# Optimization experiments

Measured on AMD Instinct MI355X. Metric: run time of the kernel, lower is better.

## Reference

```python
import jax, jax.numpy as jnp
import numpy as np

T, F, C, V, H, E, S = 256, 32, 8, 10000, 1024, 256, 512
PAD, BOS, EOS = 0, 1, 2


def setup_inputs() -> dict:
    key = jax.random.key(0)
    ks = jax.random.split(key, 16)
    sH = 1.0 / np.sqrt(H).astype(np.float32)
    inp = {
        'token_ctx': jax.random.normal(ks[0], (1, S, H), jnp.float32),
        'char_emb_w': jax.random.normal(ks[1], (V, E), jnp.float32) * 0.02,
        'enc_W_ih': jax.random.normal(ks[2], (3 * H, E), jnp.float32) * sH,
        'enc_W_hh': jax.random.normal(ks[3], (3 * H, H), jnp.float32) * sH,
        'enc_b_ih': jnp.zeros((3 * H,), jnp.float32),
        'enc_b_hh': jnp.zeros((3 * H,), jnp.float32),
        'dec_W_ih': jax.random.normal(ks[4], (3 * H, E), jnp.float32) * sH,
        'dec_W_hh': jax.random.normal(ks[5], (3 * H, H), jnp.float32) * sH,
        'dec_b_ih': jnp.zeros((3 * H,), jnp.float32),
        'dec_b_hh': jnp.zeros((3 * H,), jnp.float32),
        'out_W': jax.random.normal(ks[6], (V, H), jnp.float32) * sH,
        'out_b': jnp.zeros((V,), jnp.float32),
    }
    # (token_id, xtoken_idx, char_id) triples; every token 1..T has exactly C chars
    tok_ids = jnp.repeat(jnp.arange(1, T + 1, dtype=jnp.int32), C)
    xt_ids = jax.random.randint(ks[7], (T * C,), 0, S, jnp.int32)
    ch_ids = jax.random.randint(ks[8], (T * C,), 4, V, jnp.int32)  # avoid specials
    inp['in_sent_token_chars'] = jnp.stack([tok_ids, xt_ids, ch_ids], axis=-1)[None]
    gold = jax.random.randint(ks[9], (T * F,), 4, V, jnp.int32)  # no EOS -> full-length decode
    inp['out_chars'] = jnp.concatenate([jnp.array([BOS], jnp.int32), gold])[None]
    inp['max_tokens'] = T
    inp['max_form_len'] = F
    inp['use_teacher_forcing'] = 1
    return inp


def _gru_cell(x, h, W_ih, W_hh, b_ih, b_hh):
    # PyTorch GRU cell convention; x:[T,E], h:[T,H]
    gi = x @ W_ih.T + b_ih
    gh = h @ W_hh.T + b_hh
    i_r, i_z, i_n = jnp.split(gi, 3, axis=-1)
    h_r, h_z, h_n = jnp.split(gh, 3, axis=-1)
    r = jax.nn.sigmoid(i_r + h_r)
    z = jax.nn.sigmoid(i_z + h_z)
    n = jnp.tanh(i_n + r * h_n)
    return (1.0 - z) * n + z * h


def reference(token_ctx, char_emb_w, enc_W_ih, enc_W_hh, enc_b_ih, enc_b_hh,
              dec_W_ih, dec_W_hh, dec_b_ih, dec_b_hh, out_W, out_b,
              in_sent_token_chars, out_chars, max_tokens, max_form_len,
              use_teacher_forcing):
    Vout = out_b.shape[0]
    # ragged mask select per token id -> here every token has exactly C chars
    tc = in_sent_token_chars[0].reshape(max_tokens, -1, 3)  # [T, C, 3]
    chars = tc[:, :, 2]          # [T, C]
    xtoken_ids = tc[:, :, 1]     # [T, C]
    # enc_state = mean over the token's xtoken contexts
    h0 = jnp.mean(token_ctx[0][xtoken_ids], axis=1)  # [T, H]
    # ---- encoder GRU over the token's chars (batched over tokens) ----
    x_enc = char_emb_w[chars]  # [T, C, E]

    def enc_step(h, x):
        return _gru_cell(x, h, enc_W_ih, enc_W_hh, enc_b_ih, enc_b_hh), None

    h_enc, _ = jax.lax.scan(enc_step, h0, jnp.swapaxes(x_enc, 0, 1))  # [T, H]
    # ---- decoder GRU, max_form_len steps, teacher-forced, EOS freeze+pad ----
    # gold char for token t at step s is out_chars[0, t*F + s + 1]
    gold = out_chars[0, 1:1 + max_tokens * max_form_len].reshape(max_tokens, max_form_len)
    c0 = jnp.full((max_tokens,), out_chars[0, 0], dtype=out_chars.dtype)
    done0 = (c0 == EOS)
    last0 = jnp.zeros((max_tokens, Vout), jnp.float32)

    def dec_step(carry, g):
        h, c, done, last = carry
        x = char_emb_w[c]
        h_new = _gru_cell(x, h, dec_W_ih, dec_W_hh, dec_b_ih, dec_b_hh)
        s_new = h_new @ out_W.T + out_b
        score = jnp.where(done[:, None], last, s_new)  # pad with last score after EOS
        h = jnp.where(done[:, None], h, h_new)         # state frozen after EOS
        if use_teacher_forcing:
            c_next = g
        else:
            c_next = jnp.argmax(s_new, axis=-1).astype(c.dtype)
        done = done | (c_next == EOS)
        return (h, c_next, done, score), score

    _, scores = jax.lax.scan(dec_step, (h_enc, c0, done0, last0),
                             jnp.swapaxes(gold, 0, 1))  # [F, T, V]
    # torch.cat(dec_scores, dim=1): token-major, step-minor -> [1, T*F, V]
    return jnp.transpose(scores, (1, 0, 2)).reshape(1, max_tokens * max_form_len, Vout)
```

## Files before the change

### kernel.cpp

```cpp
#include <hip/hip_runtime.h>
#include <hip/hip_bf16.h>
#include <math.h>

#define TT   256
#define FF   32
#define CCH  8
#define VV   10000
#define HH   1024
#define EE   256
#define NG   3072
#define EOS_ID 2
#define NSTEPS 40
#define CHAIN_BLKS 256
#define CTR_INTS 512

#define LDS_B_BYTES   98304
#define LDS_GP_OFF    98304
#define LDS_STB_OFF   (98304 + 13312)
#define LDS_TOTAL     (98304 + 13312 + 2048)

typedef __attribute__((ext_vector_type(8))) short bf16x8;
typedef __attribute__((ext_vector_type(4))) float f32x4;

__device__ __forceinline__ void gload_lds16(const void* g, void* l) {
    __builtin_amdgcn_global_load_lds((const __attribute__((address_space(1))) void*)g,
                                     (__attribute__((address_space(3))) void*)l,
                                     16, 0, 0);
}

__device__ __forceinline__ float sigmf(float x) { return 1.f / (1.f + __expf(-x)); }

__global__ __launch_bounds__(256) void prep_kernel(const int* __restrict__ oc,
                                                   int* __restrict__ c_in,
                                                   unsigned char* __restrict__ done,
                                                   int* __restrict__ ctr) {
    int t = threadIdx.x;
    for (int i = t; i < CTR_INTS; i += 256) ctr[i] = 0;
    int c0 = oc[0];
    bool d = (c0 == EOS_ID);
    for (int f = 0; f < FF; ++f) {
        c_in[t * FF + f] = (f == 0) ? c0 : oc[1 + t * FF + f - 1];
        done[t * FF + f] = d ? 1 : 0;
        d = d || (oc[1 + t * FF + f] == EOS_ID);
    }
}

__global__ __launch_bounds__(256) void h0_kernel(const float* __restrict__ tctx,
                                                 const int* __restrict__ sent,
                                                 float* __restrict__ h,
                                                 __hip_bfloat16* __restrict__ A0) {
    int t = blockIdx.x;
    int tid = threadIdx.x;
    __shared__ int xt[CCH];
    if (tid < CCH) xt[tid] = sent[(t * CCH + tid) * 3 + 1];
    __syncthreads();
#pragma unroll
    for (int jj = 0; jj < 4; ++jj) {
        int j = tid + jj * 256;
        float s = 0.f;
#pragma unroll
        for (int c = 0; c < CCH; ++c) s += tctx[(size_t)xt[c] * HH + j];
        float hv = s * 0.125f;
        h[(size_t)t * HH + j] = hv;
        A0[(size_t)t * HH + j] = __float2bfloat16(hv);
    }
}

__global__ __launch_bounds__(256) void f2b_kernel(const float* __restrict__ src,
                                                  __hip_bfloat16* __restrict__ dst) {
    size_t base = ((size_t)blockIdx.x * 256 + threadIdx.x) * 4;
    float4 v = *(const float4*)(src + base);
    dst[base + 0] = __float2bfloat16(v.x);
    dst[base + 1] = __float2bfloat16(v.y);
    dst[base + 2] = __float2bfloat16(v.z);
    dst[base + 3] = __float2bfloat16(v.w);
}

__global__ __launch_bounds__(256) void build_Bg2(const float* __restrict__ Whh,
                                                 __hip_bfloat16* __restrict__ Bg) {
    int by = blockIdx.x;
    int tid = threadIdx.x;
    int jb = by / 48, rr = by % 48;
    int g = rr >> 4, jj = rr & 15;
    const float* srow = Whh + (size_t)(g * 1024 + jb * 16 + jj) * HH;
    __hip_bfloat16* drow = Bg + (size_t)by * HH;
    float4 v = *(const float4*)(srow + tid * 4);
    drow[tid * 4 + 0] = __float2bfloat16(v.x);
    drow[tid * 4 + 1] = __float2bfloat16(v.y);
    drow[tid * 4 + 2] = __float2bfloat16(v.z);
    drow[tid * 4 + 3] = __float2bfloat16(v.w);
}

template<int MODE>
__global__ __launch_bounds__(256) void gemm_pipe(const __hip_bfloat16* __restrict__ A, int lda,
                                                 const __hip_bfloat16* __restrict__ B, int ldb,
                                                 float* __restrict__ C,
                                                 const int* __restrict__ idsrc,
                                                 int NIT) {
    __shared__ __hip_bfloat16 As[4][128 * 32];
    __shared__ __hip_bfloat16 Bs[4][128 * 32];
    __shared__ int sids[128];

    const int tid = threadIdx.x;
    const int n0 = blockIdx.x * 128;
    const int m0 = blockIdx.y * 128;

    if (tid < 128) {
        int row = m0 + tid;
        int t = row & 255;
        int id;
        if (MODE == 1) { int c = row >> 8; id = idsrc[(t * CCH + c) * 3 + 2]; }
        else           { int f = row >> 8; id = idsrc[t * FF + f]; }
        sids[tid] = id;
    }
    __syncthreads();

    const int srow = tid >> 2, skq = tid & 3;
    const int l = tid & 63;
    const int w = tid >> 6;
    const int wr = (w >> 1) * 64, wc = (w & 1) * 64;
    const int fra = ((wr + (l & 15)) << 5) + ((l >> 4) << 3);
    const int frb = ((wc + (l & 15)) << 5) + ((l >> 4) << 3);

    f32x4 acc[4][4];
#pragma unroll
    for (int i = 0; i < 4; ++i)
#pragma unroll
        for (int j = 0; j < 4; ++j) acc[i][j] = (f32x4){0.f, 0.f, 0.f, 0.f};

    auto stage = [&](int slot, int it) {
        const int k0 = it * 32;
        const __hip_bfloat16* ga0 = A + (size_t)sids[srow] * lda + k0 + skq * 8;
        const __hip_bfloat16* ga1 = A + (size_t)sids[64 + srow] * lda + k0 + skq * 8;
        const __hip_bfloat16* gb0 = B + (size_t)(n0 + srow) * ldb + k0 + skq * 8;
        const __hip_bfloat16* gb1 = B + (size_t)(n0 + 64 + srow) * ldb + k0 + skq * 8;
        __hip_bfloat16* lA = &As[slot][tid * 8];
        __hip_bfloat16* lB = &Bs[slot][tid * 8];
        gload_lds16(ga0, lA);
        gload_lds16(ga1, lA + 2048);
        gload_lds16(gb0, lB);
        gload_lds16(gb1, lB + 2048);
    };

    stage(0, 0);
    stage(1, 1);

    for (int it = 0; it < NIT; ++it) {
        if (it + 2 < NIT) stage((it + 2) & 3, it + 2);
        int ahead = NIT - 1 - it; if (ahead > 2) ahead = 2;
        if (ahead >= 2)      asm volatile("s_waitcnt vmcnt(8)" ::: "memory");
        else if (ahead == 1) asm volatile("s_waitcnt vmcnt(4)" ::: "memory");
        else                 asm volatile("s_waitcnt vmcnt(0)" ::: "memory");
        __builtin_amdgcn_s_barrier();
        __builtin_amdgcn_sched_barrier(0);

        const __hip_bfloat16* cA = As[it & 3];
        const __hip_bfloat16* cB = Bs[it & 3];
        bf16x8 af[4], bfv[4];
#pragma unroll
        for (int fm = 0; fm < 4; ++fm) af[fm] = *(const bf16x8*)&cA[fra + fm * 512];
#pragma unroll
        for (int fn = 0; fn < 4; ++fn) bfv[fn] = *(const bf16x8*)&cB[frb + fn * 512];
#pragma unroll
        for (int fm = 0; fm < 4; ++fm)
#pragma unroll
            for (int fn = 0; fn < 4; ++fn)
                acc[fm][fn] = __builtin_amdgcn_mfma_f32_16x16x32_bf16(af[fm], bfv[fn], acc[fm][fn], 0, 0, 0);
    }

    const int colb = wc + (l & 15);
    const int rb   = wr + ((l >> 4) << 2);
#pragma unroll
    for (int fm = 0; fm < 4; ++fm)
#pragma unroll
        for (int fn = 0; fn < 4; ++fn)
#pragma unroll
            for (int q = 0; q < 4; ++q)
                C[(size_t)(m0 + rb + fm * 16 + q) * NG + n0 + colb + fn * 16] = acc[fm][fn][q];
}

__global__ __launch_bounds__(256, 1) void chain_kernel(
    __hip_bfloat16* Abuf0, __hip_bfloat16* Abuf1,
    const __hip_bfloat16* __restrict__ Bg_e,
    const __hip_bfloat16* __restrict__ Bg_d,
    const float* __restrict__ gi_enc, const float* __restrict__ gi_dec,
    const float* __restrict__ ebih, const float* __restrict__ ebhh,
    const float* __restrict__ dbih, const float* __restrict__ dbhh,
    const float* __restrict__ hA,
    __hip_bfloat16* __restrict__ hsb,
    const unsigned char* __restrict__ dflags,
    int* flags) {

    extern __shared__ __align__(16) char smem[];
    char* Bs = smem;
    float* gp = (float*)(smem + LDS_GP_OFF);
    __hip_bfloat16* stb = (__hip_bfloat16*)(smem + LDS_STB_OFF);

    const int tid = threadIdx.x;
    const int b = blockIdx.x;
    const int mt = b >> 6, jb = b & 63;
    const int m0 = mt * 64;
    const int jbase = jb * 16;

    const int l = tid & 63, w = tid >> 6;
    const int ji = tid & 15;
    const int rg = tid >> 4;
    const int j = jbase + ji;

    float hreg[4];
#pragma unroll
    for (int p = 0; p < 4; ++p)
        hreg[p] = hA[(size_t)(m0 + p * 16 + rg) * HH + j];

    const float e_br = ebih[j] + ebhh[j];
    const float e_bz = ebih[HH + j] + ebhh[HH + j];
    const float e_bi = ebih[2 * HH + j];
    const float e_bh = ebhh[2 * HH + j];
    const float d_br = dbih[j] + dbhh[j];
    const float d_bz = dbih[HH + j] + dbhh[HH + j];
    const float d_bi = dbih[2 * HH + j];
    const float d_bh = dbhh[2 * HH + j];

    auto stageBfull = [&](const __hip_bfloat16* Bp) {
#pragma unroll
        for (int c = 0; c < 24; ++c) {
            int chunk = c * 256 + tid;
            int row = chunk >> 7, q = chunk & 127;
            const char* src = (const char*)(Bp + (size_t)row * HH) + ((q ^ (row & 7)) << 4);
            gload_lds16(src, Bs + chunk * 16);
        }
    };

    auto ldB = [&](int nt, int ks) -> bf16x8 {
        int r = nt * 16 + (l & 15);
        int g = ks * 4 + (l >> 4);
        return *(const bf16x8*)(Bs + r * 2048 + ((g ^ (r & 7)) << 4));
    };

    float gr[4], gz[4], gn_[4];
    int dfl[4] = {0, 0, 0, 0};
#pragma unroll
    for (int p = 0; p < 4; ++p) {
        const float* gb = gi_enc + (size_t)(m0 + p * 16 + rg) * NG + j;
        asm volatile("global_load_dword %0, %1, off nt" : "=v"(gr[p])  : "v"(gb));
        asm volatile("global_load_dword %0, %1, off nt" : "=v"(gz[p])  : "v"(gb + HH));
        asm volatile("global_load_dword %0, %1, off nt" : "=v"(gn_[p]) : "v"(gb + 2 * HH));
    }

    for (int s = 0; s < NSTEPS; ++s) {
        if (s > 0) {
            if (tid < 64) {
                const int* fp = flags + (mt << 6) + l;
                long guard = 0;
                for (;;) {
                    int v;
                    asm volatile("global_load_dword %0, %1, off sc0 sc1" : "=v"(v) : "v"(fp));
                    asm volatile("s_waitcnt vmcnt(0)" ::: "memory");
                    if (__all(v >= s)) break;
                    if (++guard > (1L << 22)) break;
                    __builtin_amdgcn_s_sleep(2);
                }
            }
            __syncthreads();
        }

        if (s == 0 || s == CCH) {
            stageBfull(((s == 0) ? Bg_e : Bg_d) + (size_t)jb * 48 * HH);
            asm volatile("s_waitcnt vmcnt(0)" ::: "memory");
            __syncthreads();
        }

        const __hip_bfloat16* Ab = (s & 1) ? Abuf1 : Abuf0;
        __hip_bfloat16* An = (s & 1) ? Abuf0 : Abuf1;

        asm volatile("s_waitcnt vmcnt(0)" ::: "memory");
        const __hip_bfloat16* aptr = Ab + (size_t)(m0 + w * 16 + (l & 15)) * HH + ((l >> 4) << 3);
        bf16x8 av[32];
#pragma unroll
        for (int ks = 0; ks < 32; ++ks)
            asm volatile("global_load_dwordx4 %0, %1, off sc0 sc1"
                         : "=v"(av[ks]) : "v"(aptr + ks * 32));

        f32x4 acc[3];
        acc[0] = (f32x4){0.f, 0.f, 0.f, 0.f};
        acc[1] = (f32x4){0.f, 0.f, 0.f, 0.f};
        acc[2] = (f32x4){0.f, 0.f, 0.f, 0.f};

        bf16x8 bb[3][3];
#pragma unroll
        for (int nt = 0; nt < 3; ++nt) { bb[0][nt] = ldB(nt, 0); bb[1][nt] = ldB(nt, 1); }

#pragma unroll
        for (int ks = 0; ks < 32; ++ks) {
            if (ks + 2 < 32) {
#pragma unroll
                for (int nt = 0; nt < 3; ++nt) bb[(ks + 2) % 3][nt] = ldB(nt, ks + 2);
            }
            asm volatile("s_waitcnt vmcnt(%0)" :: "i"(31 - ks) : "memory");
            __builtin_amdgcn_sched_barrier(0);
            acc[0] = __builtin_amdgcn_mfma_f32_16x16x32_bf16(av[ks], bb[ks % 3][0], acc[0], 0, 0, 0);
            acc[1] = __builtin_amdgcn_mfma_f32_16x16x32_bf16(av[ks], bb[ks % 3][1], acc[1], 0, 0, 0);
            acc[2] = __builtin_amdgcn_mfma_f32_16x16x32_bf16(av[ks], bb[ks % 3][2], acc[2], 0, 0, 0);
        }

        {
            const int rb = w * 16 + ((l >> 4) << 2);
#pragma unroll
            for (int nt = 0; nt < 3; ++nt)
#pragma unroll
                for (int q = 0; q < 4; ++q)
                    gp[(rb + q) * 52 + nt * 16 + (l & 15)] = acc[nt][q];
        }
        __syncthreads();

        const int f = s - CCH;
        const float br_ = (s < CCH) ? e_br : d_br;
        const float bz_ = (s < CCH) ? e_bz : d_bz;
        const float bi_ = (s < CCH) ? e_bi : d_bi;
        const float bh_ = (s < CCH) ? e_bh : d_bh;
#pragma unroll
        for (int p = 0; p < 4; ++p) {
            const int tr = p * 16 + rg;
            float racc = gp[tr * 52 + ji];
            float zacc = gp[tr * 52 + 16 + ji];
            float nacc = gp[tr * 52 + 32 + ji];
            float r = sigmf(gr[p] + br_ + racc);
            float z = sigmf(gz[p] + bz_ + zacc);
            float n = tanhf(gn_[p] + bi_ + r * (nacc + bh_));
            float hold = hreg[p];
            float hv = (1.f - z) * n + z * hold;
            if (s >= CCH && dfl[p]) hv = hold;
            hreg[p] = hv;
            stb[tr * 16 + ji] = __float2bfloat16(hv);
        }
        __syncthreads();

        if (tid < 128) {
            const int row = tid >> 1, part = tid & 1;
            bf16x8 v = *(const bf16x8*)&stb[row * 16 + part * 8];
            if (s < NSTEPS - 1) {
                const __hip_bfloat16* ap = An + (size_t)(m0 + row) * HH + jbase + part * 8;
                asm volatile("global_store_dwordx4 %0, %1, off sc0 sc1"
                             :: "v"(ap), "v"(v) : "memory");
            }
            if (s >= CCH) {
                bf16x8* hp = (bf16x8*)(hsb + ((size_t)f * TT + m0 + row) * HH + jbase + part * 8);
                __builtin_nontemporal_store(v, hp);
            }
        }

        if (s < NSTEPS - 1) {
            asm volatile("s_waitcnt vmcnt(0)" ::: "memory");
            __syncthreads();
            if (tid == 0) {
                int v = s + 1;
                int* fp = flags + (mt << 6) + jb;
                asm volatile("global_store_dword %0, %1, off sc0 sc1"
                             :: "v"(fp), "v"(v) : "memory");
            }
            {
                const float* gnext = (s + 1 < CCH) ? (gi_enc + (size_t)(s + 1) * TT * NG)
                                                   : (gi_dec + (size_t)(s + 1 - CCH) * TT * NG);
#pragma unroll
                for (int p = 0; p < 4; ++p) {
                    const float* gb = gnext + (size_t)(m0 + p * 16 + rg) * NG + j;
                    asm volatile("global_load_dword %0, %1, off nt" : "=v"(gr[p])  : "v"(gb));
                    asm volatile("global_load_dword %0, %1, off nt" : "=v"(gz[p])  : "v"(gb + HH));
                    asm volatile("global_load_dword %0, %1, off nt" : "=v"(gn_[p]) : "v"(gb + 2 * HH));
                }
                if (s + 1 >= CCH) {
                    const int fnx = s + 1 - CCH;
#pragma unroll
                    for (int p = 0; p < 4; ++p) {
                        const unsigned char* dp = dflags + (size_t)(m0 + p * 16 + rg) * FF + fnx;
                        asm volatile("global_load_ubyte %0, %1, off" : "=v"(dfl[p]) : "v"(dp));
                    }
                }
            }
        }
    }
}

__global__ __launch_bounds__(256) void scores_pipe(const __hip_bfloat16* __restrict__ hsb,
                                                   const __hip_bfloat16* __restrict__ Wb,
                                                   const float* __restrict__ bout,
                                                   const int* __restrict__ oc,
                                                   float* __restrict__ out) {
    __shared__ __hip_bfloat16 As[4][128 * 32];
    __shared__ __hip_bfloat16 Bs[4][128 * 32];
    int bid = blockIdx.x;
    int sid = (bid & 7) * 632 + (bid >> 3);
    int bx = sid % 79, by = sid / 79;
    int n0 = bx * 128, m0 = by * 128;

    const int tid = threadIdx.x;
    const int l = tid & 63;
    const int w = tid >> 6;
    const int wr = (w >> 1) * 64, wc = (w & 1) * 64;
    const int srow = tid >> 2, skq = tid & 3;

    f32x4 acc[4][4];
#pragma unroll
    for (int i = 0; i < 4; ++i)
#pragma unroll
        for (int j = 0; j < 4; ++j) acc[i][j] = (f32x4){0.f, 0.f, 0.f, 0.f};

    int br0 = n0 + srow, br1 = n0 + 64 + srow;
    br0 = (br0 > VV - 1) ? VV - 1 : br0;
    br1 = (br1 > VV - 1) ? VV - 1 : br1;
    const __hip_bfloat16* gA0 = hsb + (size_t)(m0 + srow) * HH + skq * 8;
    const __hip_bfloat16* gA1 = hsb + (size_t)(m0 + 64 + srow) * HH + skq * 8;
    const __hip_bfloat16* gB0 = Wb + (size_t)br0 * HH + skq * 8;
    const __hip_bfloat16* gB1 = Wb + (size_t)br1 * HH + skq * 8;
    const int fra = ((wr + (l & 15)) << 5) + ((l >> 4) << 3);
    const int frb = ((wc + (l & 15)) << 5) + ((l >> 4) << 3);

    auto stage = [&](int slot, int it) {
        const int k0 = it * 32;
        __hip_bfloat16* lA = &As[slot][tid * 8];
        __hip_bfloat16* lB = &Bs[slot][tid * 8];
        gload_lds16(gA0 + k0, lA);
        gload_lds16(gA1 + k0, lA + 2048);
        gload_lds16(gB0 + k0, lB);
        gload_lds16(gB1 + k0, lB + 2048);
    };

    stage(0, 0);
    stage(1, 1);

    for (int it = 0; it < 32; ++it) {
        if (it + 2 < 32) stage((it + 2) & 3, it + 2);
        int ahead = 31 - it; if (ahead > 2) ahead = 2;
        if (ahead >= 2)      asm volatile("s_waitcnt vmcnt(8)" ::: "memory");
        else if (ahead == 1) asm volatile("s_waitcnt vmcnt(4)" ::: "memory");
        else                 asm volatile("s_waitcnt vmcnt(0)" ::: "memory");
        __builtin_amdgcn_s_barrier();
        __builtin_amdgcn_sched_barrier(0);

        const __hip_bfloat16* cA = As[it & 3];
        const __hip_bfloat16* cB = Bs[it & 3];
        bf16x8 af[4], bfv[4];
#pragma unroll
        for (int fm = 0; fm < 4; ++fm) af[fm] = *(const bf16x8*)&cA[fra + fm * 512];
#pragma unroll
        for (int fn = 0; fn < 4; ++fn) bfv[fn] = *(const bf16x8*)&cB[frb + fn * 512];
#pragma unroll
        for (int fm = 0; fm < 4; ++fm)
#pragma unroll
            for (int fn = 0; fn < 4; ++fn)
                acc[fm][fn] = __builtin_amdgcn_mfma_f32_16x16x32_bf16(af[fm], bfv[fn], acc[fm][fn], 0, 0, 0);
    }

    const bool zf = (oc[0] == EOS_ID);
    const int colb = wc + (l & 15);
    const int rb   = wr + ((l >> 4) << 2);
#pragma unroll
    for (int fn = 0; fn < 4; ++fn) {
        int v = n0 + colb + fn * 16;
        if (v < VV) {
            float bb = bout[v];
#pragma unroll
            for (int fm = 0; fm < 4; ++fm) {
#pragma unroll
                for (int q = 0; q < 4; ++q) {
                    int m = m0 + rb + fm * 16 + q;
                    int fo = m >> 8, t = m & 255;
                    float val = zf ? 0.f : (acc[fm][fn][q] + bb);
                    __builtin_nontemporal_store(val, &out[(size_t)(t * FF + fo) * VV + v]);
                }
            }
        }
    }
}

extern "C" void kernel_launch(void* const* d_in, const int* in_sizes, int n_in,
                              void* d_out, int out_size, void* d_ws, size_t ws_size,
                              hipStream_t stream) {
    (void)in_sizes; (void)n_in; (void)ws_size;

    const float* token_ctx = (const float*)d_in[0];
    const float* emb       = (const float*)d_in[1];
    const float* eWih      = (const float*)d_in[2];
    const float* eWhh      = (const float*)d_in[3];
    const float* ebih      = (const float*)d_in[4];
    const float* ebhh      = (const float*)d_in[5];
    const float* dWih      = (const float*)d_in[6];
    const float* dWhh      = (const float*)d_in[7];
    const float* dbih      = (const float*)d_in[8];
    const float* dbhh      = (const float*)d_in[9];
    const float* Wout      = (const float*)d_in[10];
    const float* bout      = (const float*)d_in[11];
    const int*   sent      = (const int*)d_in[12];
    const int*   ochars    = (const int*)d_in[13];
    float* out = (float*)d_out;

    char* w = (char*)d_ws;
    float* hA = (float*)w;                      w += (size_t)TT * HH * 4;
    __hip_bfloat16* Ab0 = (__hip_bfloat16*)w;   w += (size_t)TT * HH * 2;
    __hip_bfloat16* Ab1 = (__hip_bfloat16*)w;   w += (size_t)TT * HH * 2;
    __hip_bfloat16* hsb = (__hip_bfloat16*)w;   w += (size_t)FF * TT * HH * 2;
    __hip_bfloat16* Woutb = (__hip_bfloat16*)w; w += (size_t)VV * HH * 2;
    int* c_in = (int*)w;                        w += (size_t)TT * FF * 4;
    unsigned char* done = (unsigned char*)w;    w += (size_t)TT * FF;
    w = (char*)(((size_t)w + 255) & ~(size_t)255);
    int* ctr = (int*)w;                         w += (size_t)CTR_INTS * 4;

    char* tail = (char*)d_out + (size_t)out_size * 4;
    tail -= (size_t)NG * HH * 2;          __hip_bfloat16* Bg_e = (__hip_bfloat16*)tail;
    tail -= (size_t)NG * HH * 2;          __hip_bfloat16* Bg_d = (__hip_bfloat16*)tail;
    tail -= (size_t)CCH * TT * NG * 4;    float* gi_enc = (float*)tail;
    tail -= (size_t)FF * TT * NG * 4;     float* gi_dec = (float*)tail;
    tail -= (size_t)VV * EE * 2;          __hip_bfloat16* emb_bf = (__hip_bfloat16*)tail;
    tail -= (size_t)NG * EE * 2;          __hip_bfloat16* Wihb_e = (__hip_bfloat16*)tail;
    tail -= (size_t)NG * EE * 2;          __hip_bfloat16* Wihb_d = (__hip_bfloat16*)tail;

    hipFuncSetAttribute((const void*)chain_kernel,
                        hipFuncAttributeMaxDynamicSharedMemorySize, LDS_TOTAL);

    prep_kernel<<<1, 256, 0, stream>>>(ochars, c_in, done, ctr);
    h0_kernel<<<TT, 256, 0, stream>>>(token_ctx, sent, hA, Ab0);
    f2b_kernel<<<(VV * EE) / 4 / 256, 256, 0, stream>>>(emb, emb_bf);
    f2b_kernel<<<(NG * EE) / 4 / 256, 256, 0, stream>>>(eWih, Wihb_e);
    f2b_kernel<<<(NG * EE) / 4 / 256, 256, 0, stream>>>(dWih, Wihb_d);
    f2b_kernel<<<(VV * HH) / 4 / 256, 256, 0, stream>>>(Wout, Woutb);
    build_Bg2<<<NG, 256, 0, stream>>>(eWhh, Bg_e);
    build_Bg2<<<NG, 256, 0, stream>>>(dWhh, Bg_d);

    gemm_pipe<1><<<dim3(24, 16), 256, 0, stream>>>(emb_bf, EE, Wihb_e, EE, gi_enc, sent, 8);
    gemm_pipe<2><<<dim3(24, 64), 256, 0, stream>>>(emb_bf, EE, Wihb_d, EE, gi_dec, c_in, 8);

    chain_kernel<<<CHAIN_BLKS, 256, LDS_TOTAL, stream>>>(Ab0, Ab1, Bg_e, Bg_d,
                                                         gi_enc, gi_dec,
                                                         ebih, ebhh, dbih, dbhh,
                                                         hA, hsb, done, ctr);

    scores_pipe<<<5056, 256, 0, stream>>>(hsb, Woutb, bout, ochars, out);
}
```

Baseline: 697.9 us.

## Split chain-step K across waves, store input gates in bf16, move hsb store off critical path

The recurrent chain step now has each wave cover a quarter of the K dimension for all 64 rows instead of a full K for 16 rows. Partial sums go to per-wave LDS slices and are reduced during the gate computation. The precomputed input-gate projections are stored and loaded as bf16 rather than fp32, which halves that traffic. The history store to hsb is moved after the inter-block flag publish so it no longer delays the next step's signal. The cost is more LDS use, an extra reduction, and reduced precision for the input-gate terms.

```diff
diff --git a/kernel.cpp b/kernel.cpp
--- a/kernel.cpp
+++ b/kernel.cpp
@@ -14,10 +14,9 @@
 #define CHAIN_BLKS 256
 #define CTR_INTS 512
 
-#define LDS_B_BYTES   98304
 #define LDS_GP_OFF    98304
-#define LDS_STB_OFF   (98304 + 13312)
-#define LDS_TOTAL     (98304 + 13312 + 2048)
+#define LDS_STB_OFF   (98304 + 53248)
+#define LDS_TOTAL     (98304 + 53248 + 2048)
 
 typedef __attribute__((ext_vector_type(8))) short bf16x8;
 typedef __attribute__((ext_vector_type(4))) float f32x4;
@@ -94,7 +93,7 @@
 template<int MODE>
 __global__ __launch_bounds__(256) void gemm_pipe(const __hip_bfloat16* __restrict__ A, int lda,
                                                  const __hip_bfloat16* __restrict__ B, int ldb,
-                                                 float* __restrict__ C,
+                                                 __hip_bfloat16* __restrict__ Cb,
                                                  const int* __restrict__ idsrc,
                                                  int NIT) {
     __shared__ __hip_bfloat16 As[4][128 * 32];
@@ -176,14 +175,15 @@
         for (int fn = 0; fn < 4; ++fn)
 #pragma unroll
             for (int q = 0; q < 4; ++q)
-                C[(size_t)(m0 + rb + fm * 16 + q) * NG + n0 + colb + fn * 16] = acc[fm][fn][q];
+                Cb[(size_t)(m0 + rb + fm * 16 + q) * NG + n0 + colb + fn * 16] =
+                    __float2bfloat16(acc[fm][fn][q]);
 }
 
 __global__ __launch_bounds__(256, 1) void chain_kernel(
     __hip_bfloat16* Abuf0, __hip_bfloat16* Abuf1,
     const __hip_bfloat16* __restrict__ Bg_e,
     const __hip_bfloat16* __restrict__ Bg_d,
-    const float* __restrict__ gi_enc, const float* __restrict__ gi_dec,
+    const __hip_bfloat16* __restrict__ gi_enc, const __hip_bfloat16* __restrict__ gi_dec,
     const float* __restrict__ ebih, const float* __restrict__ ebhh,
     const float* __restrict__ dbih, const float* __restrict__ dbhh,
     const float* __restrict__ hA,
@@ -206,6 +206,8 @@
     const int ji = tid & 15;
     const int rg = tid >> 4;
     const int j = jbase + ji;
+    const int lrow = l & 15;
+    const int lk8  = (l >> 4) << 3;
 
     float hreg[4];
 #pragma unroll
@@ -232,19 +234,19 @@
     };
 
     auto ldB = [&](int nt, int ks) -> bf16x8 {
-        int r = nt * 16 + (l & 15);
+        int r = nt * 16 + lrow;
         int g = ks * 4 + (l >> 4);
         return *(const bf16x8*)(Bs + r * 2048 + ((g ^ (r & 7)) << 4));
     };
 
-    float gr[4], gz[4], gn_[4];
+    unsigned int gru[4], gzu[4], gnu[4];
     int dfl[4] = {0, 0, 0, 0};
 #pragma unroll
     for (int p = 0; p < 4; ++p) {
-        const float* gb = gi_enc + (size_t)(m0 + p * 16 + rg) * NG + j;
-        asm volatile("global_load_dword %0, %1, off nt" : "=v"(gr[p])  : "v"(gb));
-        asm volatile("global_load_dword %0, %1, off nt" : "=v"(gz[p])  : "v"(gb + HH));
-        asm volatile("global_load_dword %0, %1, off nt" : "=v"(gn_[p]) : "v"(gb + 2 * HH));
+        const __hip_bfloat16* gb = gi_enc + (size_t)(m0 + p * 16 + rg) * NG + j;
+        asm volatile("global_load_ushort %0, %1, off nt" : "=v"(gru[p]) : "v"(gb));
+        asm volatile("global_load_ushort %0, %1, off nt" : "=v"(gzu[p]) : "v"(gb + HH));
+        asm volatile("global_load_ushort %0, %1, off nt" : "=v"(gnu[p]) : "v"(gb + 2 * HH));
     }
 
     for (int s = 0; s < NSTEPS; ++s) {
@@ -274,42 +276,56 @@
         __hip_bfloat16* An = (s & 1) ? Abuf0 : Abuf1;
 
         asm volatile("s_waitcnt vmcnt(0)" ::: "memory");
-        const __hip_bfloat16* aptr = Ab + (size_t)(m0 + w * 16 + (l & 15)) * HH + ((l >> 4) << 3);
-        bf16x8 av[32];
-#pragma unroll
-        for (int ks = 0; ks < 32; ++ks)
-            asm volatile("global_load_dwordx4 %0, %1, off sc0 sc1"
-                         : "=v"(av[ks]) : "v"(aptr + ks * 32));
-
-        f32x4 acc[3];
-        acc[0] = (f32x4){0.f, 0.f, 0.f, 0.f};
-        acc[1] = (f32x4){0.f, 0.f, 0.f, 0.f};
-        acc[2] = (f32x4){0.f, 0.f, 0.f, 0.f};
-
+        const __hip_bfloat16* ap0 = Ab + (size_t)(m0 + 0 * 16 + lrow) * HH + w * 256 + lk8;
+        const __hip_bfloat16* ap1 = Ab + (size_t)(m0 + 1 * 16 + lrow) * HH + w * 256 + lk8;
+        const __hip_bfloat16* ap2 = Ab + (size_t)(m0 + 2 * 16 + lrow) * HH + w * 256 + lk8;
+        const __hip_bfloat16* ap3 = Ab + (size_t)(m0 + 3 * 16 + lrow) * HH + w * 256 + lk8;
+
+        bf16x8 av[8][4];
+#pragma unroll
+        for (int ksl = 0; ksl < 8; ++ksl) {
+            asm volatile("global_load_dwordx4 %0, %1, off sc0 sc1" : "=v"(av[ksl][0]) : "v"(ap0 + ksl * 32));
+            asm volatile("global_load_dwordx4 %0, %1, off sc0 sc1" : "=v"(av[ksl][1]) : "v"(ap1 + ksl * 32));
+            asm volatile("global_load_dwordx4 %0, %1, off sc0 sc1" : "=v"(av[ksl][2]) : "v"(ap2 + ksl * 32));
+            asm volatile("global_load_dwordx4 %0, %1, off sc0 sc1" : "=v"(av[ksl][3]) : "v"(ap3 + ksl * 32));
+        }
+
+        f32x4 acc[4][3];
+#pragma unroll
+        for (int m = 0; m < 4; ++m)
+#pragma unroll
+            for (int nt = 0; nt < 3; ++nt) acc[m][nt] = (f32x4){0.f, 0.f, 0.f, 0.f};
+
+        const int kbase = w * 8;
         bf16x8 bb[3][3];
 #pragma unroll
-        for (int nt = 0; nt < 3; ++nt) { bb[0][nt] = ldB(nt, 0); bb[1][nt] = ldB(nt, 1); }
-
-#pragma unroll
-        for (int ks = 0; ks < 32; ++ks) {
-            if (ks + 2 < 32) {
-#pragma unroll
-                for (int nt = 0; nt < 3; ++nt) bb[(ks + 2) % 3][nt] = ldB(nt, ks + 2);
-            }
-            asm volatile("s_waitcnt vmcnt(%0)" :: "i"(31 - ks) : "memory");
+        for (int nt = 0; nt < 3; ++nt) { bb[0][nt] = ldB(nt, kbase); bb[1][nt] = ldB(nt, kbase + 1); }
+
+#pragma unroll
+        for (int ksl = 0; ksl < 8; ++ksl) {
+            if (ksl + 2 < 8) {
+#pragma unroll
+                for (int nt = 0; nt < 3; ++nt) bb[(ksl + 2) % 3][nt] = ldB(nt, kbase + ksl + 2);
+            }
+            asm volatile("s_waitcnt vmcnt(%0)" :: "i"(28 - 4 * ksl) : "memory");
             __builtin_amdgcn_sched_barrier(0);
-            acc[0] = __builtin_amdgcn_mfma_f32_16x16x32_bf16(av[ks], bb[ks % 3][0], acc[0], 0, 0, 0);
-            acc[1] = __builtin_amdgcn_mfma_f32_16x16x32_bf16(av[ks], bb[ks % 3][1], acc[1], 0, 0, 0);
-            acc[2] = __builtin_amdgcn_mfma_f32_16x16x32_bf16(av[ks], bb[ks % 3][2], acc[2], 0, 0, 0);
+#pragma unroll
+            for (int m = 0; m < 4; ++m)
+#pragma unroll
+                for (int nt = 0; nt < 3; ++nt)
+                    acc[m][nt] = __builtin_amdgcn_mfma_f32_16x16x32_bf16(av[ksl][m], bb[ksl % 3][nt], acc[m][nt], 0, 0, 0);
         }
 
         {
-            const int rb = w * 16 + ((l >> 4) << 2);
-#pragma unroll
-            for (int nt = 0; nt < 3; ++nt)
-#pragma unroll
-                for (int q = 0; q < 4; ++q)
-                    gp[(rb + q) * 52 + nt * 16 + (l & 15)] = acc[nt][q];
+            float* gpw = gp + w * (64 * 52);
+            const int rbase = (l >> 4) << 2;
+#pragma unroll
+            for (int m = 0; m < 4; ++m)
+#pragma unroll
+                for (int nt = 0; nt < 3; ++nt)
+#pragma unroll
+                    for (int q = 0; q < 4; ++q)
+                        gpw[(m * 16 + rbase + q) * 52 + nt * 16 + lrow] = acc[m][nt][q];
         }
         __syncthreads();
 
@@ -321,12 +337,20 @@
 #pragma unroll
         for (int p = 0; p < 4; ++p) {
             const int tr = p * 16 + rg;
-            float racc = gp[tr * 52 + ji];
-            float zacc = gp[tr * 52 + 16 + ji];
-            float nacc = gp[tr * 52 + 32 + ji];
-            float r = sigmf(gr[p] + br_ + racc);
-            float z = sigmf(gz[p] + bz_ + zacc);
-            float n = tanhf(gn_[p] + bi_ + r * (nacc + bh_));
+            float racc = 0.f, zacc = 0.f, nacc = 0.f;
+#pragma unroll
+            for (int ww = 0; ww < 4; ++ww) {
+                const float* g = gp + ww * (64 * 52) + tr * 52;
+                racc += g[ji];
+                zacc += g[16 + ji];
+                nacc += g[32 + ji];
+            }
+            float grf = __uint_as_float(gru[p] << 16);
+            float gzf = __uint_as_float(gzu[p] << 16);
+            float gnf = __uint_as_float(gnu[p] << 16);
+            float r = sigmf(grf + br_ + racc);
+            float z = sigmf(gzf + bz_ + zacc);
+            float n = tanhf(gnf + bi_ + r * (nacc + bh_));
             float hold = hreg[p];
             float hv = (1.f - z) * n + z * hold;
             if (s >= CCH && dfl[p]) hv = hold;
@@ -335,21 +359,14 @@
         }
         __syncthreads();
 
-        if (tid < 128) {
-            const int row = tid >> 1, part = tid & 1;
-            bf16x8 v = *(const bf16x8*)&stb[row * 16 + part * 8];
-            if (s < NSTEPS - 1) {
+        if (s < NSTEPS - 1) {
+            if (tid < 128) {
+                const int row = tid >> 1, part = tid & 1;
+                bf16x8 v = *(const bf16x8*)&stb[row * 16 + part * 8];
                 const __hip_bfloat16* ap = An + (size_t)(m0 + row) * HH + jbase + part * 8;
                 asm volatile("global_store_dwordx4 %0, %1, off sc0 sc1"
                              :: "v"(ap), "v"(v) : "memory");
             }
-            if (s >= CCH) {
-                bf16x8* hp = (bf16x8*)(hsb + ((size_t)f * TT + m0 + row) * HH + jbase + part * 8);
-                __builtin_nontemporal_store(v, hp);
-            }
-        }
-
-        if (s < NSTEPS - 1) {
             asm volatile("s_waitcnt vmcnt(0)" ::: "memory");
             __syncthreads();
             if (tid == 0) {
@@ -358,23 +375,29 @@
                 asm volatile("global_store_dword %0, %1, off sc0 sc1"
                              :: "v"(fp), "v"(v) : "memory");
             }
-            {
-                const float* gnext = (s + 1 < CCH) ? (gi_enc + (size_t)(s + 1) * TT * NG)
-                                                   : (gi_dec + (size_t)(s + 1 - CCH) * TT * NG);
+        }
+        if (s >= CCH && tid < 128) {
+            const int row = tid >> 1, part = tid & 1;
+            bf16x8 v = *(const bf16x8*)&stb[row * 16 + part * 8];
+            bf16x8* hp = (bf16x8*)(hsb + ((size_t)f * TT + m0 + row) * HH + jbase + part * 8);
+            __builtin_nontemporal_store(v, hp);
+        }
+        if (s < NSTEPS - 1) {
+            const __hip_bfloat16* gnext = (s + 1 < CCH) ? (gi_enc + (size_t)(s + 1) * TT * NG)
+                                                        : (gi_dec + (size_t)(s + 1 - CCH) * TT * NG);
+#pragma unroll
+            for (int p = 0; p < 4; ++p) {
+                const __hip_bfloat16* gb = gnext + (size_t)(m0 + p * 16 + rg) * NG + j;
+                asm volatile("global_load_ushort %0, %1, off nt" : "=v"(gru[p]) : "v"(gb));
+                asm volatile("global_load_ushort %0, %1, off nt" : "=v"(gzu[p]) : "v"(gb + HH));
+                asm volatile("global_load_ushort %0, %1, off nt" : "=v"(gnu[p]) : "v"(gb + 2 * HH));
+            }
+            if (s + 1 >= CCH) {
+                const int fnx = s + 1 - CCH;
 #pragma unroll
                 for (int p = 0; p < 4; ++p) {
-                    const float* gb = gnext + (size_t)(m0 + p * 16 + rg) * NG + j;
-                    asm volatile("global_load_dword %0, %1, off nt" : "=v"(gr[p])  : "v"(gb));
-                    asm volatile("global_load_dword %0, %1, off nt" : "=v"(gz[p])  : "v"(gb + HH));
-                    asm volatile("global_load_dword %0, %1, off nt" : "=v"(gn_[p]) : "v"(gb + 2 * HH));
-                }
-                if (s + 1 >= CCH) {
-                    const int fnx = s + 1 - CCH;
-#pragma unroll
-                    for (int p = 0; p < 4; ++p) {
-                        const unsigned char* dp = dflags + (size_t)(m0 + p * 16 + rg) * FF + fnx;
-                        asm volatile("global_load_ubyte %0, %1, off" : "=v"(dfl[p]) : "v"(dp));
-                    }
+                    const unsigned char* dp = dflags + (size_t)(m0 + p * 16 + rg) * FF + fnx;
+                    asm volatile("global_load_ubyte %0, %1, off" : "=v"(dfl[p]) : "v"(dp));
                 }
             }
         }
@@ -508,8 +531,8 @@
     char* tail = (char*)d_out + (size_t)out_size * 4;
     tail -= (size_t)NG * HH * 2;          __hip_bfloat16* Bg_e = (__hip_bfloat16*)tail;
     tail -= (size_t)NG * HH * 2;          __hip_bfloat16* Bg_d = (__hip_bfloat16*)tail;
-    tail -= (size_t)CCH * TT * NG * 4;    float* gi_enc = (float*)tail;
-    tail -= (size_t)FF * TT * NG * 4;     float* gi_dec = (float*)tail;
+    tail -= (size_t)CCH * TT * NG * 2;    __hip_bfloat16* gi_enc = (__hip_bfloat16*)tail;
+    tail -= (size_t)FF * TT * NG * 2;     __hip_bfloat16* gi_dec = (__hip_bfloat16*)tail;
     tail -= (size_t)VV * EE * 2;          __hip_bfloat16* emb_bf = (__hip_bfloat16*)tail;
     tail -= (size_t)NG * EE * 2;          __hip_bfloat16* Wihb_e = (__hip_bfloat16*)tail;
     tail -= (size_t)NG * EE * 2;          __hip_bfloat16* Wihb_d = (__hip_bfloat16*)tail;
```

Result: no change. 693.5 us (-0.6%).
